# Performance work log

Hardware: AMD Instinct MI355X
Metric: run time of the kernel (lower is better)

Reference implementation:

```python
import jax, jax.numpy as jnp
import numpy as np

B, T, S, E, H, K, V = 64, 100, 400, 512, 1024, 512, 34


def _lstm_cell(x, h, c, w_ih, w_hh, b_ih, b_hh):
    # torch.nn.LSTMCell: gates ordered i, f, g, o
    gates = x @ w_ih.T + b_ih + h @ w_hh.T + b_hh
    i, f, g, o = jnp.split(gates, 4, axis=-1)
    c_new = jax.nn.sigmoid(f) * c + jax.nn.sigmoid(i) * jnp.tanh(g)
    h_new = jax.nn.sigmoid(o) * jnp.tanh(c_new)
    return h_new, c_new


def setup_inputs() -> dict:
    key = jax.random.key(0)
    ks = jax.random.split(key, 24)
    s = 0.02
    d = {
        "labels": jax.random.randint(ks[0], (B, T), 0, V),
        "keys": jax.random.normal(ks[1], (S, B, K), dtype=jnp.float32),
        "values": jax.random.normal(ks[2], (S, B, K), dtype=jnp.float32),
        "emb": jax.random.normal(ks[3], (V, E), dtype=jnp.float32) * s,
        # cell 0: input E+K, cells 1-2: input H
        "w_ih0": jax.random.normal(ks[4], (4 * H, E + K), dtype=jnp.float32) * s,
        "w_hh0": jax.random.normal(ks[5], (4 * H, H), dtype=jnp.float32) * s,
        "b_ih0": jnp.zeros((4 * H,), jnp.float32),
        "b_hh0": jnp.zeros((4 * H,), jnp.float32),
        "w_ih1": jax.random.normal(ks[6], (4 * H, H), dtype=jnp.float32) * s,
        "w_hh1": jax.random.normal(ks[7], (4 * H, H), dtype=jnp.float32) * s,
        "b_ih1": jnp.zeros((4 * H,), jnp.float32),
        "b_hh1": jnp.zeros((4 * H,), jnp.float32),
        "w_ih2": jax.random.normal(ks[8], (4 * H, H), dtype=jnp.float32) * s,
        "w_hh2": jax.random.normal(ks[9], (4 * H, H), dtype=jnp.float32) * s,
        "b_ih2": jnp.zeros((4 * H,), jnp.float32),
        "b_hh2": jnp.zeros((4 * H,), jnp.float32),
        "w_proj": jax.random.normal(ks[10], (K, H), dtype=jnp.float32) * s,
        "b_proj": jnp.zeros((K,), jnp.float32),
        "w_score": jax.random.normal(ks[11], (V, 2 * K), dtype=jnp.float32) * s,
        "b_score": jnp.zeros((V,), jnp.float32),
        "h0": jnp.zeros((1, H), jnp.float32),
    }
    return d


def reference(labels, keys, values, emb,
              w_ih0, w_hh0, b_ih0, b_hh0,
              w_ih1, w_hh1, b_ih1, b_hh1,
              w_ih2, w_hh2, b_ih2, b_hh2,
              w_proj, b_proj, w_score, b_score, h0):
    bsz = labels.shape[0]
    h = jnp.repeat(h0, bsz, axis=0)                 # [B, H]
    context0 = h @ w_proj.T + b_proj                # [B, K]
    keys_p = jnp.transpose(keys, (1, 2, 0))          # [B, K, S]
    values_p = jnp.transpose(values, (1, 0, 2))      # [B, S, K]
    xs = jnp.transpose(emb[labels], (1, 0, 2))       # [T, B, E] (teacher forcing)

    def step(carry, x_t):
        h1, c1, h2, c2, h3, c3, ctx = carry
        dec_in = jnp.concatenate([x_t, ctx], axis=-1)            # [B, E+K]
        h1, c1 = _lstm_cell(dec_in, h1, c1, w_ih0, w_hh0, b_ih0, b_hh0)
        h2, c2 = _lstm_cell(h1, h2, c2, w_ih1, w_hh1, b_ih1, b_hh1)
        h3, c3 = _lstm_cell(h2, h3, c3, w_ih2, w_hh2, b_ih2, b_hh2)
        q = h3 @ w_proj.T + b_proj                               # [B, K]
        energy = jnp.einsum('bk,bks->bs', q, keys_p)             # [B, S]
        attn = jax.nn.softmax(energy, axis=-1)
        ctx = jnp.einsum('bs,bsk->bk', attn, values_p)           # [B, K]
        score = jnp.concatenate([q, ctx], axis=-1) @ w_score.T + b_score  # [B, V]
        return (h1, c1, h2, c2, h3, c3, ctx), (score, attn)

    init = (h, h, h, h, h, h, context0)
    _, (scores, attns) = jax.lax.scan(step, init, xs)
    all_predictions = jnp.transpose(scores, (1, 0, 2))  # [B, T, V]
    all_attention = jnp.transpose(attns, (1, 0, 2))     # [B, T, S]
    return all_predictions, all_attention
```

## Files before the change

kernel.cpp:

```cpp
#include <hip/hip_runtime.h>
#include <cstdint>
#include <cstddef>

#define Bz 64
#define Td 100
#define Sd 400
#define Ed 512
#define Hd 1024
#define Kd 512
#define Vd 34

typedef __attribute__((ext_vector_type(8))) short short8v;
typedef __attribute__((ext_vector_type(8))) unsigned short ushort8v;
typedef __attribute__((ext_vector_type(4))) float floatx4;

__device__ __forceinline__ float sigmoidf_(float x) {
    return 1.0f / (1.0f + __expf(-x));
}
__device__ __forceinline__ float tanhf_(float x) {
    float e = __expf(-2.0f * fabsf(x));
    float r = (1.0f - e) / (1.0f + e);
    return copysignf(r, x);
}
__device__ __forceinline__ unsigned short f2bf(float x) {
    unsigned int u = __float_as_uint(x);
    unsigned int r = (u + 0x7fffu + ((u >> 16) & 1u)) >> 16;
    return (unsigned short)r;
}
__device__ __forceinline__ float bf2f(unsigned short h) {
    return __uint_as_float(((unsigned int)h) << 16);
}

__global__ __launch_bounds__(256) void pack_w_kernel(
    const float* __restrict__ w, unsigned short* __restrict__ hi,
    unsigned short* __restrict__ lo, int n4)
{
    int i = blockIdx.x * 256 + threadIdx.x;
    if (i >= n4) return;
    float4 v = ((const float4*)w)[i];
    float f[4] = {v.x, v.y, v.z, v.w};
    unsigned short h[4], l[4];
    #pragma unroll
    for (int e = 0; e < 4; ++e) {
        h[e] = f2bf(f[e]);
        l[e] = f2bf(f[e] - bf2f(h[e]));
    }
    ushort4 hv = {h[0], h[1], h[2], h[3]};
    ushort4 lv = {l[0], l[1], l[2], l[3]};
    ((ushort4*)hi)[i] = hv;
    ((ushort4*)lo)[i] = lv;
}

__global__ __launch_bounds__(256) void gemm_cell_mfma(
    const float* __restrict__ src0, const int* __restrict__ labels, int t,
    const float* __restrict__ ctx, const float* __restrict__ h_prev,
    const unsigned short* __restrict__ wih_hi, const unsigned short* __restrict__ wih_lo,
    const unsigned short* __restrict__ whh_hi, const unsigned short* __restrict__ whh_lo,
    float* __restrict__ gpart, int mode)
{
    __shared__ unsigned short xs[64 * 264];
    const int tid  = threadIdx.x;
    const int w    = tid >> 6;
    const int lane = tid & 63;
    const int quad = lane >> 4;
    const int l16  = lane & 15;
    const int nt   = blockIdx.x & 31;
    const int ks   = blockIdx.x >> 5;
    const int nA   = nt * 128 + w * 16;
    const int nB   = nA + 64;

    const unsigned short* whi = (ks < 4) ? wih_hi : whh_hi;
    const unsigned short* wlo = (ks < 4) ? wih_lo : whh_lo;
    const int kcol0 = (ks & 3) * 256;

    floatx4 zero = {0.f, 0.f, 0.f, 0.f};
    floatx4 accA[4] = {zero, zero, zero, zero};
    floatx4 accB[4] = {zero, zero, zero, zero};

    for (int kc = 0; kc < 2; ++kc) {
        __syncthreads();
        #pragma unroll
        for (int it = 0; it < 4; ++it) {
            int p = it * 256 + tid;
            int r = p >> 4;
            int g = p & 15;
            int kg = kcol0 + kc * 128 + g * 8;
            const float* srow;
            if (mode == 0) {
                if (ks < 2)      srow = src0 + (size_t)labels[r * Td + t] * Ed + kg;
                else if (ks < 4) srow = ctx + r * Kd + (kg - 512);
                else             srow = h_prev + r * Hd + kg;
            } else {
                if (ks < 4)      srow = src0 + r * Hd + kg;
                else             srow = h_prev + r * Hd + kg;
            }
            float4 v0 = *(const float4*)(srow);
            float4 v1 = *(const float4*)(srow + 4);
            float f[8] = {v0.x, v0.y, v0.z, v0.w, v1.x, v1.y, v1.z, v1.w};
            ushort8v H, L;
            #pragma unroll
            for (int e = 0; e < 8; ++e) {
                unsigned short h = f2bf(f[e]);
                H[e] = h;
                L[e] = f2bf(f[e] - bf2f(h));
            }
            unsigned short* dst = xs + r * 264 + g * 16;
            *(ushort8v*)dst       = H;
            *(ushort8v*)(dst + 8) = L;
        }
        __syncthreads();

        int kcol = kcol0 + kc * 128 + quad * 8;
        size_t rA = ((size_t)(nA + l16)) * 1024 + kcol;
        size_t rB = ((size_t)(nB + l16)) * 1024 + kcol;
        short8v bAh = *(const short8v*)(whi + rA);
        short8v bAl = *(const short8v*)(wlo + rA);
        short8v bBh = *(const short8v*)(whi + rB);
        short8v bBl = *(const short8v*)(wlo + rB);
        #pragma unroll
        for (int kk = 0; kk < 4; ++kk) {
            short8v cAh = bAh, cAl = bAl, cBh = bBh, cBl = bBl;
            if (kk < 3) {
                bAh = *(const short8v*)(whi + rA + 32 * (kk + 1));
                bAl = *(const short8v*)(wlo + rA + 32 * (kk + 1));
                bBh = *(const short8v*)(whi + rB + 32 * (kk + 1));
                bBl = *(const short8v*)(wlo + rB + 32 * (kk + 1));
            }
            #pragma unroll
            for (int mf = 0; mf < 4; ++mf) {
                const unsigned short* ar = xs + (mf * 16 + l16) * 264 + (kk * 4 + quad) * 16;
                short8v ah = *(const short8v*)ar;
                short8v al = *(const short8v*)(ar + 8);
                accA[mf] = __builtin_amdgcn_mfma_f32_16x16x32_bf16(ah, cAh, accA[mf], 0, 0, 0);
                accA[mf] = __builtin_amdgcn_mfma_f32_16x16x32_bf16(al, cAh, accA[mf], 0, 0, 0);
                accA[mf] = __builtin_amdgcn_mfma_f32_16x16x32_bf16(ah, cAl, accA[mf], 0, 0, 0);
                accB[mf] = __builtin_amdgcn_mfma_f32_16x16x32_bf16(ah, cBh, accB[mf], 0, 0, 0);
                accB[mf] = __builtin_amdgcn_mfma_f32_16x16x32_bf16(al, cBh, accB[mf], 0, 0, 0);
                accB[mf] = __builtin_amdgcn_mfma_f32_16x16x32_bf16(ah, cBl, accB[mf], 0, 0, 0);
            }
        }
    }

    #pragma unroll
    for (int mf = 0; mf < 4; ++mf) {
        int m = mf * 16 + quad * 4;
        float* gA = gpart + ((size_t)ks * 64 + m) * 4096 + nA + l16;
        float* gB = gpart + ((size_t)ks * 64 + m) * 4096 + nB + l16;
        #pragma unroll
        for (int reg = 0; reg < 4; ++reg) {
            gA[(size_t)reg * 4096] = accA[mf][reg];
            gB[(size_t)reg * 4096] = accB[mf][reg];
        }
    }
}

__global__ __launch_bounds__(256) void gemm_cell(
    const float* __restrict__ src0,
    const int* __restrict__ labels, int t,
    const float* __restrict__ ctx,
    const float* __restrict__ h_prev,
    const float* __restrict__ w_ih, const float* __restrict__ w_hh,
    float* __restrict__ gpart, int mode)
{
    __shared__ float lds[32 * 132];
    const int tid = threadIdx.x;
    const int bq  = tid & 15;
    const int jl  = tid >> 4;
    const int bid = blockIdx.x;
    const int jg  = bid & 63;
    const int ks  = (bid >> 6) & 3;
    const int bh  = bid >> 8;
    const int j   = jg * 16 + jl;
    const int b0  = bh * 32;

    const float* wsrc = (ks < 2) ? w_ih : w_hh;
    const int koff = (ks & 1) * 512;
    const float* w0 = wsrc + ((size_t)j)          * 1024 + koff;
    const float* w1 = wsrc + ((size_t)(1024 + j)) * 1024 + koff;
    const float* w2 = wsrc + ((size_t)(2048 + j)) * 1024 + koff;
    const float* w3 = wsrc + ((size_t)(3072 + j)) * 1024 + koff;

    float acc00 = 0.f, acc01 = 0.f, acc02 = 0.f, acc03 = 0.f;
    float acc10 = 0.f, acc11 = 0.f, acc12 = 0.f, acc13 = 0.f;

    for (int sub = 0; sub < 4; ++sub) {
        __syncthreads();
        #pragma unroll
        for (int it = 0; it < 4; ++it) {
            int idx = (it << 8) + tid;
            int r   = idx >> 5;
            int c4  = (idx & 31) << 2;
            int b   = b0 + r;
            const float* src;
            if (mode == 0) {
                if (ks == 0)      src = src0 + (size_t)labels[b * Td + t] * Ed + (sub << 7) + c4;
                else if (ks == 1) src = ctx + b * Kd + (sub << 7) + c4;
                else              src = h_prev + b * Hd + ((ks - 2) << 9) + (sub << 7) + c4;
            } else {
                if (ks < 2)       src = src0 + b * Hd + (ks << 9) + (sub << 7) + c4;
                else              src = h_prev + b * Hd + ((ks - 2) << 9) + (sub << 7) + c4;
            }
            float4 v = *(const float4*)src;
            float* d = lds + r * 132 + c4;
            d[0] = v.x; d[1] = v.y; d[2] = v.z; d[3] = v.w;
        }
        __syncthreads();

        const float* wp0 = w0 + (sub << 7);
        const float* wp1 = w1 + (sub << 7);
        const float* wp2 = w2 + (sub << 7);
        const float* wp3 = w3 + (sub << 7);
        const float* l0  = lds + bq * 132;
        const float* l1  = lds + (bq + 16) * 132;
        #pragma unroll 4
        for (int k4 = 0; k4 < 32; ++k4) {
            float4 wv0 = *(const float4*)(wp0 + (k4 << 2));
            float4 wv1 = *(const float4*)(wp1 + (k4 << 2));
            float4 wv2 = *(const float4*)(wp2 + (k4 << 2));
            float4 wv3 = *(const float4*)(wp3 + (k4 << 2));
            float4 a0  = *(const float4*)(l0 + (k4 << 2));
            float4 a1  = *(const float4*)(l1 + (k4 << 2));
            acc00 += a0.x*wv0.x; acc00 += a0.y*wv0.y; acc00 += a0.z*wv0.z; acc00 += a0.w*wv0.w;
            acc01 += a0.x*wv1.x; acc01 += a0.y*wv1.y; acc01 += a0.z*wv1.z; acc01 += a0.w*wv1.w;
            acc02 += a0.x*wv2.x; acc02 += a0.y*wv2.y; acc02 += a0.z*wv2.z; acc02 += a0.w*wv2.w;
            acc03 += a0.x*wv3.x; acc03 += a0.y*wv3.y; acc03 += a0.z*wv3.z; acc03 += a0.w*wv3.w;
            acc10 += a1.x*wv0.x; acc10 += a1.y*wv0.y; acc10 += a1.z*wv0.z; acc10 += a1.w*wv0.w;
            acc11 += a1.x*wv1.x; acc11 += a1.y*wv1.y; acc11 += a1.z*wv1.z; acc11 += a1.w*wv1.w;
            acc12 += a1.x*wv2.x; acc12 += a1.y*wv2.y; acc12 += a1.z*wv2.z; acc12 += a1.w*wv2.w;
            acc13 += a1.x*wv3.x; acc13 += a1.y*wv3.y; acc13 += a1.z*wv3.z; acc13 += a1.w*wv3.w;
        }
    }

    const size_t rowA = ((size_t)ks * 64 + b0 + bq) * 4096;
    const size_t rowB = ((size_t)ks * 64 + b0 + bq + 16) * 4096;
    gpart[rowA + 0 * 1024 + j] = acc00;
    gpart[rowA + 1 * 1024 + j] = acc01;
    gpart[rowA + 2 * 1024 + j] = acc02;
    gpart[rowA + 3 * 1024 + j] = acc03;
    gpart[rowB + 0 * 1024 + j] = acc10;
    gpart[rowB + 1 * 1024 + j] = acc11;
    gpart[rowB + 2 * 1024 + j] = acc12;
    gpart[rowB + 3 * 1024 + j] = acc13;
}

__global__ __launch_bounds__(256) void combine_cell(
    const float* __restrict__ gpart,
    const float* __restrict__ b_ih, const float* __restrict__ b_hh,
    float* c, float* __restrict__ h, int nsl)
{
    int el = blockIdx.x * 256 + threadIdx.x;
    int b = el >> 10, j = el & 1023;
    float g[4];
    #pragma unroll
    for (int gi = 0; gi < 4; ++gi)
        g[gi] = b_ih[gi * 1024 + j] + b_hh[gi * 1024 + j];
    for (int ksi = 0; ksi < nsl; ++ksi) {
        const float* row = gpart + ((size_t)ksi * 64 + b) * 4096 + j;
        #pragma unroll
        for (int gi = 0; gi < 4; ++gi)
            g[gi] += row[gi * 1024];
    }
    float ig = sigmoidf_(g[0]);
    float fg = sigmoidf_(g[1]);
    float gg = tanhf_(g[2]);
    float og = sigmoidf_(g[3]);
    float cn = fg * c[el] + ig * gg;
    c[el] = cn;
    h[el] = og * tanhf_(cn);
}

__global__ __launch_bounds__(256) void gemm_q(
    const float* __restrict__ h3, const float* __restrict__ w_proj,
    float* __restrict__ qpart)
{
    __shared__ float lds[32 * 132];
    const int tid = threadIdx.x;
    const int bq = tid & 15, nl = tid >> 4;
    const int bid = blockIdx.x;
    const int ng = bid & 31, ks = (bid >> 5) & 3, bh = bid >> 7;
    const int n = ng * 16 + nl;
    const int b0 = bh * 32;
    const float* wp = w_proj + (size_t)n * 1024 + (ks << 8);

    float acc0 = 0.f, acc1 = 0.f;
    for (int sub = 0; sub < 2; ++sub) {
        __syncthreads();
        #pragma unroll
        for (int it = 0; it < 4; ++it) {
            int idx = (it << 8) + tid;
            int r = idx >> 5, c4 = (idx & 31) << 2;
            float4 v = *(const float4*)(h3 + (size_t)(b0 + r) * 1024 + (ks << 8) + (sub << 7) + c4);
            float* d = lds + r * 132 + c4;
            d[0] = v.x; d[1] = v.y; d[2] = v.z; d[3] = v.w;
        }
        __syncthreads();
        const float* l0 = lds + bq * 132;
        const float* l1 = lds + (bq + 16) * 132;
        const float* wq = wp + (sub << 7);
        #pragma unroll 4
        for (int k4 = 0; k4 < 32; ++k4) {
            float4 wv = *(const float4*)(wq + (k4 << 2));
            float4 a0 = *(const float4*)(l0 + (k4 << 2));
            float4 a1 = *(const float4*)(l1 + (k4 << 2));
            acc0 += a0.x*wv.x; acc0 += a0.y*wv.y; acc0 += a0.z*wv.z; acc0 += a0.w*wv.w;
            acc1 += a1.x*wv.x; acc1 += a1.y*wv.y; acc1 += a1.z*wv.z; acc1 += a1.w*wv.w;
        }
    }
    qpart[((size_t)ks * 64 + b0 + bq) * 512 + n]      = acc0;
    qpart[((size_t)ks * 64 + b0 + bq + 16) * 512 + n] = acc1;
}

__global__ __launch_bounds__(256) void energy_kernel(
    const float* __restrict__ qpart, const float* __restrict__ b_proj,
    const float* __restrict__ keys, const float* __restrict__ values,
    float* __restrict__ attn, int t,
    float* __restrict__ u_part, float* __restrict__ m_part, float* __restrict__ z_part)
{
    __shared__ float qs[4 * 132];
    __shared__ float es[64];
    __shared__ float ps[64];
    __shared__ float mz[1];
    const int tid = threadIdx.x;
    const int b   = blockIdx.x >> 3;
    const int ch  = blockIdx.x & 7;

    for (int k = tid; k < 512; k += 256) {
        float s = b_proj[k];
        #pragma unroll
        for (int ksi = 0; ksi < 4; ++ksi)
            s += qpart[((size_t)ksi * 64 + b) * 512 + k];
        qs[(k >> 7) * 132 + (k & 127)] = s;
    }
    __syncthreads();

    if (tid < 200) {
        int sl = tid >> 2, part = tid & 3;
        int s = ch * 50 + sl;
        const float* kr = keys + ((size_t)s * Bz + b) * Kd + part * 128;
        const float* qp = qs + part * 132;
        float e = 0.f;
        #pragma unroll 8
        for (int i4 = 0; i4 < 32; ++i4) {
            float4 kv = *(const float4*)(kr + (i4 << 2));
            e += qp[(i4 << 2) + 0] * kv.x;
            e += qp[(i4 << 2) + 1] * kv.y;
            e += qp[(i4 << 2) + 2] * kv.z;
            e += qp[(i4 << 2) + 3] * kv.w;
        }
        e += __shfl_down(e, 1);
        e += __shfl_down(e, 2);
        if (part == 0) es[sl] = e;
    }
    __syncthreads();
    if (tid == 0) {
        float m = -1e30f;
        for (int i = 0; i < 50; ++i) m = fmaxf(m, es[i]);
        mz[0] = m;
    }
    __syncthreads();
    float m = mz[0];
    if (tid < 50) {
        float p = __expf(es[tid] - m);
        ps[tid] = p;
        attn[(size_t)b * (Td * Sd) + t * Sd + ch * 50 + tid] = p;
    }
    __syncthreads();
    if (tid == 0) {
        float z = 0.f;
        for (int i = 0; i < 50; ++i) z += ps[i];
        m_part[b * 8 + ch] = m;
        z_part[b * 8 + ch] = z;
    }
    float u0 = 0.f, u1 = 0.f;
    const float* vbase = values + ((size_t)(ch * 50) * Bz + b) * Kd;
    for (int s = 0; s < 50; ++s) {
        const float* vr = vbase + (size_t)s * Bz * Kd;
        float p = ps[s];
        u0 += p * vr[tid];
        u1 += p * vr[tid + 256];
    }
    u_part[((b << 3) + ch) * 512 + tid]       = u0;
    u_part[((b << 3) + ch) * 512 + tid + 256] = u1;
}

__global__ __launch_bounds__(256) void finalize_kernel(
    const float* __restrict__ qpart, const float* __restrict__ b_proj,
    const float* __restrict__ u_part,
    const float* __restrict__ m_part, const float* __restrict__ z_part,
    float* __restrict__ ctx, float* __restrict__ attn, float* __restrict__ pred,
    const float* __restrict__ w_score, const float* __restrict__ b_score, int t)
{
    __shared__ float fc[8];
    __shared__ float qs[512];
    __shared__ float cs[512];
    const int tid = threadIdx.x;
    const int b = blockIdx.x;

    if (tid == 0) {
        float M = -1e30f;
        for (int c = 0; c < 8; ++c) M = fmaxf(M, m_part[b * 8 + c]);
        float f[8];
        float Z = 0.f;
        for (int c = 0; c < 8; ++c) {
            f[c] = __expf(m_part[b * 8 + c] - M);
            Z += z_part[b * 8 + c] * f[c];
        }
        float inv = 1.0f / Z;
        for (int c = 0; c < 8; ++c) fc[c] = f[c] * inv;
    }
    __syncthreads();

    for (int k = tid; k < 512; k += 256) {
        float s = b_proj[k];
        #pragma unroll
        for (int ksi = 0; ksi < 4; ++ksi)
            s += qpart[((size_t)ksi * 64 + b) * 512 + k];
        qs[k] = s;
        float acc = 0.f;
        #pragma unroll
        for (int c = 0; c < 8; ++c)
            acc += u_part[((b << 3) + c) * 512 + k] * fc[c];
        ctx[b * Kd + k] = acc;
        cs[k] = acc;
    }
    for (int s = tid; s < Sd; s += 256) {
        attn[(size_t)b * (Td * Sd) + t * Sd + s] *= fc[s / 50];
    }
    __syncthreads();

    if (tid < 136) {
        int v = tid >> 2, part = tid & 3;
        const float* wr = w_score + (size_t)v * 1024 + part * 256;
        const float* src = (part < 2) ? (qs + part * 256) : (cs + (part - 2) * 256);
        float acc = 0.f;
        #pragma unroll 8
        for (int i = 0; i < 256; ++i) acc += src[i] * wr[i];
        acc += __shfl_down(acc, 1);
        acc += __shfl_down(acc, 2);
        if (part == 0) pred[(size_t)b * (Td * Vd) + t * Vd + v] = acc + b_score[v];
    }
}

__global__ void init_states(const float* __restrict__ h0,
    float* h1, float* h2, float* h3, float* c1, float* c2, float* c3)
{
    int idx = blockIdx.x * 256 + threadIdx.x;
    int arr = idx >> 16;
    int off = idx & 65535;
    float v = h0[off & 1023];
    float* p;
    switch (arr) {
        case 0: p = h1; break;
        case 1: p = h2; break;
        case 2: p = h3; break;
        case 3: p = c1; break;
        case 4: p = c2; break;
        default: p = c3; break;
    }
    p[off] = v;
}

__global__ void init_ctx(const float* __restrict__ h0, const float* __restrict__ w_proj,
                         const float* __restrict__ b_proj, float* __restrict__ ctx)
{
    int k = blockIdx.x * 256 + threadIdx.x;
    float acc = b_proj[k];
    const float* wr = w_proj + (size_t)k * 1024;
    for (int j = 0; j < 1024; ++j) acc += h0[j] * wr[j];
    for (int b = 0; b < Bz; ++b) ctx[b * Kd + k] = acc;
}

extern "C" void kernel_launch(void* const* d_in, const int* in_sizes, int n_in,
                              void* d_out, int out_size, void* d_ws, size_t ws_size,
                              hipStream_t stream)
{
    (void)in_sizes; (void)n_in; (void)out_size;
    const int*   labels = (const int*)d_in[0];
    const float* keys   = (const float*)d_in[1];
    const float* values = (const float*)d_in[2];
    const float* emb    = (const float*)d_in[3];
    const float* w_ih0  = (const float*)d_in[4];
    const float* w_hh0  = (const float*)d_in[5];
    const float* b_ih0  = (const float*)d_in[6];
    const float* b_hh0  = (const float*)d_in[7];
    const float* w_ih1  = (const float*)d_in[8];
    const float* w_hh1  = (const float*)d_in[9];
    const float* b_ih1  = (const float*)d_in[10];
    const float* b_hh1  = (const float*)d_in[11];
    const float* w_ih2  = (const float*)d_in[12];
    const float* w_hh2  = (const float*)d_in[13];
    const float* b_ih2  = (const float*)d_in[14];
    const float* b_hh2  = (const float*)d_in[15];
    const float* w_proj = (const float*)d_in[16];
    const float* b_proj = (const float*)d_in[17];
    const float* w_score= (const float*)d_in[18];
    const float* b_score= (const float*)d_in[19];
    const float* h0     = (const float*)d_in[20];

    float* ws = (float*)d_ws;
    float* h1 = ws + 0;
    float* h2 = ws + 65536;
    float* h3 = ws + 131072;
    float* c1 = ws + 196608;
    float* c2 = ws + 262144;
    float* c3 = ws + 327680;
    float* ctx = ws + 393216;
    float* gpart = ws + 425984;
    float* qpart = ws + 2523136;
    float* u_part = ws + 2654208;
    float* m_part = ws + 2916352;
    float* z_part = ws + 2916864;
    unsigned short* wp_base = (unsigned short*)(ws + 2917376);
    const size_t PLANE = (size_t)4096 * 1024;
    const size_t NEED  = (size_t)2917376 * 4 + 12 * PLANE * 2;
    const bool fast = (ws_size >= NEED);

    unsigned short* Whi[3][2]; unsigned short* Wlo[3][2];
    const float* Wsrc[3][2] = {{w_ih0, w_hh0}, {w_ih1, w_hh1}, {w_ih2, w_hh2}};
    for (int c = 0; c < 3; ++c)
        for (int p = 0; p < 2; ++p) {
            Whi[c][p] = wp_base + ((size_t)(c * 2 + p) * 2 + 0) * PLANE;
            Wlo[c][p] = wp_base + ((size_t)(c * 2 + p) * 2 + 1) * PLANE;
        }

    float* pred = (float*)d_out;
    float* attn = (float*)d_out + (size_t)Bz * Td * Vd;

    if (fast) {
        const int n4 = (int)(PLANE / 4);
        for (int c = 0; c < 3; ++c)
            for (int p = 0; p < 2; ++p)
                pack_w_kernel<<<(n4 + 255) / 256, 256, 0, stream>>>(
                    Wsrc[c][p], Whi[c][p], Wlo[c][p], n4);
    }

    init_states<<<1536, 256, 0, stream>>>(h0, h1, h2, h3, c1, c2, c3);
    init_ctx<<<2, 256, 0, stream>>>(h0, w_proj, b_proj, ctx);

    const float* bih[3] = {b_ih0, b_ih1, b_ih2};
    const float* bhh[3] = {b_hh0, b_hh1, b_hh2};
    float* hs[3] = {h1, h2, h3};
    float* cs_[3] = {c1, c2, c3};

    for (int t = 0; t < Td; ++t) {
        for (int cell = 0; cell < 3; ++cell) {
            const float* x  = (cell == 0) ? emb : hs[cell - 1];
            const int mode  = (cell == 0) ? 0 : 1;
            if (fast) {
                gemm_cell_mfma<<<256, 256, 0, stream>>>(
                    x, labels, t, ctx, hs[cell],
                    Whi[cell][0], Wlo[cell][0], Whi[cell][1], Wlo[cell][1],
                    gpart, mode);
                combine_cell<<<256, 256, 0, stream>>>(gpart, bih[cell], bhh[cell],
                                                      cs_[cell], hs[cell], 8);
            } else {
                gemm_cell<<<512, 256, 0, stream>>>(
                    x, labels, t, ctx, hs[cell],
                    Wsrc[cell][0], Wsrc[cell][1], gpart, mode);
                combine_cell<<<256, 256, 0, stream>>>(gpart, bih[cell], bhh[cell],
                                                      cs_[cell], hs[cell], 4);
            }
        }
        gemm_q<<<256, 256, 0, stream>>>(h3, w_proj, qpart);
        energy_kernel<<<512, 256, 0, stream>>>(qpart, b_proj, keys, values, attn, t,
                                               u_part, m_part, z_part);
        finalize_kernel<<<64, 256, 0, stream>>>(qpart, b_proj, u_part, m_part, z_part,
                                                ctx, attn, pred, w_score, b_score, t);
    }
}
```

Before: 9.498 ms.

## Pre-split activations into bf16 hi/lo in producers and widen MFMA gate blocks to 512 threads

The kernels that produce hidden states and context (combine_cell, finalize, init kernels) now also write bf16 hi/lo copies, and the embedding table is packed once. The gate GEMM loads these packed activations directly instead of reading fp32 and converting per block. The GEMM block also grows to 512 threads, with each wave covering 32 rows instead of 64, to add parallelism and cut per-wave register use. This removes repeated conversion work across the 256 blocks per cell, in exchange for extra stores in the combine and finalize kernels and more workspace.

```diff
diff --git a/kernel.cpp b/kernel.cpp
--- a/kernel.cpp
+++ b/kernel.cpp
@@ -51,9 +51,11 @@
     ((ushort4*)lo)[i] = lv;
 }
 
-__global__ __launch_bounds__(256) void gemm_cell_mfma(
-    const float* __restrict__ src0, const int* __restrict__ labels, int t,
-    const float* __restrict__ ctx, const float* __restrict__ h_prev,
+__global__ __launch_bounds__(512) void gemm_cell_mfma(
+    const unsigned short* __restrict__ x_hi, const unsigned short* __restrict__ x_lo,
+    const int* __restrict__ labels, int t,
+    const unsigned short* __restrict__ ctx_hi, const unsigned short* __restrict__ ctx_lo,
+    const unsigned short* __restrict__ hp_hi, const unsigned short* __restrict__ hp_lo,
     const unsigned short* __restrict__ wih_hi, const unsigned short* __restrict__ wih_lo,
     const unsigned short* __restrict__ whh_hi, const unsigned short* __restrict__ whh_lo,
     float* __restrict__ gpart, int mode)
@@ -66,44 +68,38 @@
     const int l16  = lane & 15;
     const int nt   = blockIdx.x & 31;
     const int ks   = blockIdx.x >> 5;
-    const int nA   = nt * 128 + w * 16;
-    const int nB   = nA + 64;
+    const int mh   = w >> 2;
+    const int nA   = nt * 128 + (w & 3) * 32;
+    const int nB   = nA + 16;
 
     const unsigned short* whi = (ks < 4) ? wih_hi : whh_hi;
     const unsigned short* wlo = (ks < 4) ? wih_lo : whh_lo;
     const int kcol0 = (ks & 3) * 256;
 
     floatx4 zero = {0.f, 0.f, 0.f, 0.f};
-    floatx4 accA[4] = {zero, zero, zero, zero};
-    floatx4 accB[4] = {zero, zero, zero, zero};
+    floatx4 accA[2] = {zero, zero};
+    floatx4 accB[2] = {zero, zero};
 
     for (int kc = 0; kc < 2; ++kc) {
         __syncthreads();
         #pragma unroll
-        for (int it = 0; it < 4; ++it) {
-            int p = it * 256 + tid;
+        for (int it = 0; it < 2; ++it) {
+            int p = it * 512 + tid;
             int r = p >> 4;
             int g = p & 15;
             int kg = kcol0 + kc * 128 + g * 8;
-            const float* srow;
+            const unsigned short *shi, *slo;
+            size_t idx;
             if (mode == 0) {
-                if (ks < 2)      srow = src0 + (size_t)labels[r * Td + t] * Ed + kg;
-                else if (ks < 4) srow = ctx + r * Kd + (kg - 512);
-                else             srow = h_prev + r * Hd + kg;
+                if (ks < 2)      { idx = (size_t)labels[r * Td + t] * Ed + kg; shi = x_hi;  slo = x_lo; }
+                else if (ks < 4) { idx = (size_t)r * Kd + (kg - 512);          shi = ctx_hi; slo = ctx_lo; }
+                else             { idx = (size_t)r * Hd + kg;                  shi = hp_hi; slo = hp_lo; }
             } else {
-                if (ks < 4)      srow = src0 + r * Hd + kg;
-                else             srow = h_prev + r * Hd + kg;
+                if (ks < 4)      { idx = (size_t)r * Hd + kg;                  shi = x_hi;  slo = x_lo; }
+                else             { idx = (size_t)r * Hd + kg;                  shi = hp_hi; slo = hp_lo; }
             }
-            float4 v0 = *(const float4*)(srow);
-            float4 v1 = *(const float4*)(srow + 4);
-            float f[8] = {v0.x, v0.y, v0.z, v0.w, v1.x, v1.y, v1.z, v1.w};
-            ushort8v H, L;
-            #pragma unroll
-            for (int e = 0; e < 8; ++e) {
-                unsigned short h = f2bf(f[e]);
-                H[e] = h;
-                L[e] = f2bf(f[e] - bf2f(h));
-            }
+            ushort8v H = *(const ushort8v*)(shi + idx);
+            ushort8v L = *(const ushort8v*)(slo + idx);
             unsigned short* dst = xs + r * 264 + g * 16;
             *(ushort8v*)dst       = H;
             *(ushort8v*)(dst + 8) = L;
@@ -127,8 +123,8 @@
                 bBl = *(const short8v*)(wlo + rB + 32 * (kk + 1));
             }
             #pragma unroll
-            for (int mf = 0; mf < 4; ++mf) {
-                const unsigned short* ar = xs + (mf * 16 + l16) * 264 + (kk * 4 + quad) * 16;
+            for (int mf = 0; mf < 2; ++mf) {
+                const unsigned short* ar = xs + (mh * 32 + mf * 16 + l16) * 264 + (kk * 4 + quad) * 16;
                 short8v ah = *(const short8v*)ar;
                 short8v al = *(const short8v*)(ar + 8);
                 accA[mf] = __builtin_amdgcn_mfma_f32_16x16x32_bf16(ah, cAh, accA[mf], 0, 0, 0);
@@ -142,8 +138,8 @@
     }
 
     #pragma unroll
-    for (int mf = 0; mf < 4; ++mf) {
-        int m = mf * 16 + quad * 4;
+    for (int mf = 0; mf < 2; ++mf) {
+        int m = mh * 32 + mf * 16 + quad * 4;
         float* gA = gpart + ((size_t)ks * 64 + m) * 4096 + nA + l16;
         float* gB = gpart + ((size_t)ks * 64 + m) * 4096 + nB + l16;
         #pragma unroll
@@ -246,7 +242,8 @@
 __global__ __launch_bounds__(256) void combine_cell(
     const float* __restrict__ gpart,
     const float* __restrict__ b_ih, const float* __restrict__ b_hh,
-    float* c, float* __restrict__ h, int nsl)
+    float* c, float* __restrict__ h,
+    unsigned short* __restrict__ h_hi, unsigned short* __restrict__ h_lo, int nsl)
 {
     int el = blockIdx.x * 256 + threadIdx.x;
     int b = el >> 10, j = el & 1023;
@@ -266,7 +263,13 @@
     float og = sigmoidf_(g[3]);
     float cn = fg * c[el] + ig * gg;
     c[el] = cn;
-    h[el] = og * tanhf_(cn);
+    float hv = og * tanhf_(cn);
+    h[el] = hv;
+    if (h_hi) {
+        unsigned short hh = f2bf(hv);
+        h_hi[el] = hh;
+        h_lo[el] = f2bf(hv - bf2f(hh));
+    }
 }
 
 __global__ __launch_bounds__(256) void gemm_q(
@@ -387,7 +390,9 @@
     const float* __restrict__ qpart, const float* __restrict__ b_proj,
     const float* __restrict__ u_part,
     const float* __restrict__ m_part, const float* __restrict__ z_part,
-    float* __restrict__ ctx, float* __restrict__ attn, float* __restrict__ pred,
+    float* __restrict__ ctx,
+    unsigned short* __restrict__ ctx_hi, unsigned short* __restrict__ ctx_lo,
+    float* __restrict__ attn, float* __restrict__ pred,
     const float* __restrict__ w_score, const float* __restrict__ b_score, int t)
 {
     __shared__ float fc[8];
@@ -421,6 +426,11 @@
         for (int c = 0; c < 8; ++c)
             acc += u_part[((b << 3) + c) * 512 + k] * fc[c];
         ctx[b * Kd + k] = acc;
+        if (ctx_hi) {
+            unsigned short hh = f2bf(acc);
+            ctx_hi[b * Kd + k] = hh;
+            ctx_lo[b * Kd + k] = f2bf(acc - bf2f(hh));
+        }
         cs[k] = acc;
     }
     for (int s = tid; s < Sd; s += 256) {
@@ -442,7 +452,10 @@
 }
 
 __global__ void init_states(const float* __restrict__ h0,
-    float* h1, float* h2, float* h3, float* c1, float* c2, float* c3)
+    float* h1, float* h2, float* h3, float* c1, float* c2, float* c3,
+    unsigned short* h1h, unsigned short* h1l,
+    unsigned short* h2h, unsigned short* h2l,
+    unsigned short* h3h, unsigned short* h3l, int do_pack)
 {
     int idx = blockIdx.x * 256 + threadIdx.x;
     int arr = idx >> 16;
@@ -458,16 +471,29 @@
         default: p = c3; break;
     }
     p[off] = v;
+    if (do_pack && arr < 3) {
+        unsigned short* ph = (arr == 0) ? h1h : (arr == 1) ? h2h : h3h;
+        unsigned short* pl = (arr == 0) ? h1l : (arr == 1) ? h2l : h3l;
+        unsigned short hh = f2bf(v);
+        ph[off] = hh;
+        pl[off] = f2bf(v - bf2f(hh));
+    }
 }
 
 __global__ void init_ctx(const float* __restrict__ h0, const float* __restrict__ w_proj,
-                         const float* __restrict__ b_proj, float* __restrict__ ctx)
+                         const float* __restrict__ b_proj, float* __restrict__ ctx,
+                         unsigned short* ctx_hi, unsigned short* ctx_lo, int do_pack)
 {
     int k = blockIdx.x * 256 + threadIdx.x;
     float acc = b_proj[k];
     const float* wr = w_proj + (size_t)k * 1024;
     for (int j = 0; j < 1024; ++j) acc += h0[j] * wr[j];
-    for (int b = 0; b < Bz; ++b) ctx[b * Kd + k] = acc;
+    unsigned short hh = f2bf(acc);
+    unsigned short ll = f2bf(acc - bf2f(hh));
+    for (int b = 0; b < Bz; ++b) {
+        ctx[b * Kd + k] = acc;
+        if (do_pack) { ctx_hi[b * Kd + k] = hh; ctx_lo[b * Kd + k] = ll; }
+    }
 }
 
 extern "C" void kernel_launch(void* const* d_in, const int* in_sizes, int n_in,
@@ -510,18 +536,25 @@
     float* u_part = ws + 2654208;
     float* m_part = ws + 2916352;
     float* z_part = ws + 2916864;
-    unsigned short* wp_base = (unsigned short*)(ws + 2917376);
+
+    unsigned short* us_base = (unsigned short*)(ws + 2917376);
     const size_t PLANE = (size_t)4096 * 1024;
-    const size_t NEED  = (size_t)2917376 * 4 + 12 * PLANE * 2;
-    const bool fast = (ws_size >= NEED);
-
     unsigned short* Whi[3][2]; unsigned short* Wlo[3][2];
     const float* Wsrc[3][2] = {{w_ih0, w_hh0}, {w_ih1, w_hh1}, {w_ih2, w_hh2}};
     for (int c = 0; c < 3; ++c)
         for (int p = 0; p < 2; ++p) {
-            Whi[c][p] = wp_base + ((size_t)(c * 2 + p) * 2 + 0) * PLANE;
-            Wlo[c][p] = wp_base + ((size_t)(c * 2 + p) * 2 + 1) * PLANE;
-        }
+            Whi[c][p] = us_base + ((size_t)(c * 2 + p) * 2 + 0) * PLANE;
+            Wlo[c][p] = us_base + ((size_t)(c * 2 + p) * 2 + 1) * PLANE;
+        }
+    unsigned short* act = us_base + 12 * PLANE;
+    unsigned short* h1h = act;            unsigned short* h1l = act + 65536;
+    unsigned short* h2h = act + 131072;   unsigned short* h2l = act + 196608;
+    unsigned short* h3h = act + 262144;   unsigned short* h3l = act + 327680;
+    unsigned short* ctxh = act + 393216;  unsigned short* ctxl = act + 425984;
+    unsigned short* embh = act + 458752;  unsigned short* embl = act + 476160;
+    const size_t US_TOTAL = 12 * PLANE + 458752 + 2 * 17408;
+    const size_t NEED = (size_t)2917376 * 4 + US_TOTAL * 2;
+    const bool fast = (ws_size >= NEED);
 
     float* pred = (float*)d_out;
     float* attn = (float*)d_out + (size_t)Bz * Td * Vd;
@@ -532,39 +565,47 @@
             for (int p = 0; p < 2; ++p)
                 pack_w_kernel<<<(n4 + 255) / 256, 256, 0, stream>>>(
                     Wsrc[c][p], Whi[c][p], Wlo[c][p], n4);
-    }
-
-    init_states<<<1536, 256, 0, stream>>>(h0, h1, h2, h3, c1, c2, c3);
-    init_ctx<<<2, 256, 0, stream>>>(h0, w_proj, b_proj, ctx);
+        pack_w_kernel<<<(4352 + 255) / 256, 256, 0, stream>>>(emb, embh, embl, 4352);
+    }
+
+    init_states<<<1536, 256, 0, stream>>>(h0, h1, h2, h3, c1, c2, c3,
+                                          h1h, h1l, h2h, h2l, h3h, h3l, fast ? 1 : 0);
+    init_ctx<<<2, 256, 0, stream>>>(h0, w_proj, b_proj, ctx, ctxh, ctxl, fast ? 1 : 0);
 
     const float* bih[3] = {b_ih0, b_ih1, b_ih2};
     const float* bhh[3] = {b_hh0, b_hh1, b_hh2};
     float* hs[3] = {h1, h2, h3};
     float* cs_[3] = {c1, c2, c3};
+    unsigned short* hh_[3] = {h1h, h2h, h3h};
+    unsigned short* hl_[3] = {h1l, h2l, h3l};
 
     for (int t = 0; t < Td; ++t) {
         for (int cell = 0; cell < 3; ++cell) {
-            const float* x  = (cell == 0) ? emb : hs[cell - 1];
-            const int mode  = (cell == 0) ? 0 : 1;
             if (fast) {
-                gemm_cell_mfma<<<256, 256, 0, stream>>>(
-                    x, labels, t, ctx, hs[cell],
+                const unsigned short* xh = (cell == 0) ? embh : hh_[cell - 1];
+                const unsigned short* xl = (cell == 0) ? embl : hl_[cell - 1];
+                gemm_cell_mfma<<<256, 512, 0, stream>>>(
+                    xh, xl, labels, t, ctxh, ctxl, hh_[cell], hl_[cell],
                     Whi[cell][0], Wlo[cell][0], Whi[cell][1], Wlo[cell][1],
-                    gpart, mode);
+                    gpart, (cell == 0) ? 0 : 1);
                 combine_cell<<<256, 256, 0, stream>>>(gpart, bih[cell], bhh[cell],
-                                                      cs_[cell], hs[cell], 8);
+                                                      cs_[cell], hs[cell],
+                                                      hh_[cell], hl_[cell], 8);
             } else {
+                const float* x = (cell == 0) ? emb : hs[cell - 1];
                 gemm_cell<<<512, 256, 0, stream>>>(
                     x, labels, t, ctx, hs[cell],
-                    Wsrc[cell][0], Wsrc[cell][1], gpart, mode);
+                    Wsrc[cell][0], Wsrc[cell][1], gpart, (cell == 0) ? 0 : 1);
                 combine_cell<<<256, 256, 0, stream>>>(gpart, bih[cell], bhh[cell],
-                                                      cs_[cell], hs[cell], 4);
+                                                      cs_[cell], hs[cell],
+                                                      nullptr, nullptr, 4);
             }
         }
         gemm_q<<<256, 256, 0, stream>>>(h3, w_proj, qpart);
         energy_kernel<<<512, 256, 0, stream>>>(qpart, b_proj, keys, values, attn, t,
                                                u_part, m_part, z_part);
         finalize_kernel<<<64, 256, 0, stream>>>(qpart, b_proj, u_part, m_part, z_part,
-                                                ctx, attn, pred, w_score, b_score, t);
-    }
-}
+                                                ctx, fast ? ctxh : nullptr, fast ? ctxl : nullptr,
+                                                attn, pred, w_score, b_score, t);
+    }
+}
```

After: 9.512 ms. Within noise of the previous version (+0.1%).
